# Optimization experiments

Hardware: AMD Instinct MI355X
Metric: run time of the kernel (lower is better)

The kernel has to match this reference:

```python
import jax, jax.numpy as jnp
import numpy as np

T, B, E, H = 2048, 4, 1024, 16
D = E // H  # head_dim = 64
SCALING = D ** -0.5


def setup_inputs() -> dict:
    key = jax.random.key(0)
    ks = jax.random.split(key, 5)
    w_scale = (2.0 / (E + E)) ** 0.5  # xavier_uniform-ish std
    return {
        "query": jax.random.normal(ks[0], (T, B, E), dtype=jnp.float32),
        "q_weight": jax.random.normal(ks[1], (E, E), dtype=jnp.float32) * w_scale,
        "k_weight": jax.random.normal(ks[2], (E, E), dtype=jnp.float32) * w_scale,
        "v_weight": jax.random.normal(ks[3], (E, E), dtype=jnp.float32) * w_scale,
        "out_proj_weight": jax.random.normal(ks[4], (E, E), dtype=jnp.float32) * w_scale,
        "q_bias": jnp.zeros((E,), dtype=jnp.float32),
        "k_bias": jnp.zeros((E,), dtype=jnp.float32),
        "v_bias": jnp.zeros((E,), dtype=jnp.float32),
        "out_proj_bias": jnp.zeros((E,), dtype=jnp.float32),
    }


def reference(query, q_weight, k_weight, v_weight, out_proj_weight,
              q_bias, k_bias, v_bias, out_proj_bias):
    # Linear projections: y = x @ W.T + b  (torch F.linear convention)
    q = jnp.einsum('tbe,fe->tbf', query, q_weight) + q_bias
    k = jnp.einsum('tbe,fe->tbf', query, k_weight) + k_bias
    v = jnp.einsum('tbe,fe->tbf', query, v_weight) + v_bias
    # split heads: [T, B, H, D]
    q = q.reshape(T, B, H, D) * SCALING
    k = k.reshape(T, B, H, D)
    v = v.reshape(T, B, H, D)
    # attention scores [B, H, T, T] over keys s
    scores = jnp.einsum('tbhd,sbhd->bhts', q, k)
    attn = jax.nn.softmax(scores, axis=-1)
    # context [T, B, H, D] -> [T, B, E]
    ctx = jnp.einsum('bhts,sbhd->tbhd', attn, v).reshape(T, B, E)
    # output projection
    out = jnp.einsum('tbe,fe->tbf', ctx, out_proj_weight) + out_proj_bias
    return out
```

## Files before the change

kernel.cpp:

```cpp
#include <hip/hip_runtime.h>
#include <hip/hip_bf16.h>
#include <stdint.h>

#define T_   2048
#define B_   4
#define E_   1024
#define H_   16
#define D_   64
#define M_   8192
#define KDIM 1024

using bf16 = __hip_bfloat16;
typedef __attribute__((ext_vector_type(8)))  short bf16x8;
typedef __attribute__((ext_vector_type(4)))  float f32x4;
typedef __attribute__((ext_vector_type(16))) float f32x16;

#define QK_SCALE 0.180336880f

#if __has_builtin(__builtin_amdgcn_exp2f)
#define EXP2F(x) __builtin_amdgcn_exp2f(x)
#else
#define EXP2F(x) exp2f(x)
#endif

__device__ __forceinline__ void gload_lds16(const void* g, void* l) {
  __builtin_amdgcn_global_load_lds(
      (const __attribute__((address_space(1))) void*)g,
      (__attribute__((address_space(3))) void*)l, 16, 0, 0);
}

__device__ __forceinline__ uint32_t pack_bf16(float lo, float hi) {
  union { __hip_bfloat162 h2; uint32_t u; } cv;
  cv.h2 = __float22bfloat162_rn(float2{lo, hi});
  return cv.u;
}

__device__ __forceinline__ void plswap(uint32_t& a, uint32_t& b) {
#if __has_builtin(__builtin_amdgcn_permlane32_swap)
  typedef __attribute__((ext_vector_type(2))) unsigned int u32x2_t;
  u32x2_t r = __builtin_amdgcn_permlane32_swap(a, b, false, false);
  a = r[0]; b = r[1];
#else
  asm volatile("v_permlane32_swap_b32 %0, %1" : "+v"(a), "+v"(b));
#endif
}
__device__ __forceinline__ float comb_add32(float x) {
  union { float f; uint32_t u; } a, b; a.f = x; b.f = x;
  plswap(a.u, b.u);
  return a.f + b.f;
}

__global__ void k_cvt_all(const float* __restrict__ X,
                          const float* __restrict__ Wq, const float* __restrict__ Wk,
                          const float* __restrict__ Wv, const float* __restrict__ Wo,
                          bf16* __restrict__ Xb,
                          bf16* __restrict__ Wqb, bf16* __restrict__ Wkb,
                          bf16* __restrict__ Wvb, bf16* __restrict__ Wob) {
  int id = blockIdx.x;
  const float* src; bf16* dst; int base;
  if (id < 8192) { src = X; dst = Xb; base = id; }
  else {
    int w = (id - 8192) >> 10;
    base = (id - 8192) & 1023;
    src = (w == 0) ? Wq : (w == 1) ? Wk : (w == 2) ? Wv : Wo;
    dst = (w == 0) ? Wqb : (w == 1) ? Wkb : (w == 2) ? Wvb : Wob;
  }
  int i = base * 256 + threadIdx.x;
  float4 v = reinterpret_cast<const float4*>(src)[i];
  bf16* d = dst + (size_t)i * 4;
  d[0] = __float2bfloat16(v.x);
  d[1] = __float2bfloat16(v.y);
  d[2] = __float2bfloat16(v.z);
  d[3] = __float2bfloat16(v.w);
}

__device__ __forceinline__ void gemm_tile_body(
    const bf16* __restrict__ A, const bf16* __restrict__ Bw,
    int bm, int bn, bf16* sA, bf16* sB, f32x4 (&acc)[4][4])
{
  const int t    = threadIdx.x;
  const int wave = t >> 6;
  const int lane = t & 63;
  const int l15  = lane & 15, l4 = lane >> 4;
  const int wr = wave >> 1, wc = wave & 1;
  const int srow = t >> 3;
  const int sg   = t & 7;

  for (int k0 = 0; k0 < KDIM; k0 += 64) {
#pragma unroll
    for (int rd = 0; rd < 4; ++rd) {
      int row = rd * 32 + srow;
      const bf16* src = A + (size_t)(bm * 128 + row) * KDIM + k0 + ((sg ^ (row & 7)) * 8);
      gload_lds16(src, sA + rd * 2048 + wave * 512);
    }
#pragma unroll
    for (int rd = 0; rd < 4; ++rd) {
      int row = rd * 32 + srow;
      const bf16* src = Bw + (size_t)(bn * 128 + row) * KDIM + k0 + ((sg ^ (row & 7)) * 8);
      gload_lds16(src, sB + rd * 2048 + wave * 512);
    }
    __syncthreads();

#pragma unroll
    for (int kk = 0; kk < 2; ++kk) {
      bf16x8 af[4], bfr[4];
#pragma unroll
      for (int m = 0; m < 4; ++m) {
        int row = wr * 64 + m * 16 + l15;
        int ch  = (l4 + kk * 4) ^ (row & 7);
        af[m] = *(const bf16x8*)(sA + row * 64 + ch * 8);
      }
#pragma unroll
      for (int n = 0; n < 4; ++n) {
        int row = wc * 64 + n * 16 + l15;
        int ch  = (l4 + kk * 4) ^ (row & 7);
        bfr[n] = *(const bf16x8*)(sB + row * 64 + ch * 8);
      }
#pragma unroll
      for (int m = 0; m < 4; ++m)
#pragma unroll
        for (int n = 0; n < 4; ++n)
          acc[m][n] = __builtin_amdgcn_mfma_f32_16x16x32_bf16(af[m], bfr[n], acc[m][n], 0, 0, 0);
    }
    __syncthreads();
  }
}

__global__ __launch_bounds__(256, 3) void k_gemm_qkv(
    const bf16* __restrict__ A,
    const bf16* __restrict__ Wq, const bf16* __restrict__ Wk, const bf16* __restrict__ Wv,
    const float* __restrict__ bq, const float* __restrict__ bk, const float* __restrict__ bv,
    bf16* __restrict__ outQ)
{
  __shared__ bf16 sA[128 * 64];
  __shared__ bf16 sB[128 * 64];
  const int bid = blockIdx.x;
  const int swz = (bid & 7) * 192 + (bid >> 3);
  const int bm = swz & 63;
  const int bn = swz >> 6;
  const int which = bn >> 3;
  const int bnn = bn & 7;
  const bf16* Bw = (which == 0) ? Wq : (which == 1) ? Wk : Wv;
  const float* bias = (which == 0) ? bq : (which == 1) ? bk : bv;
  const float scale = (which == 0) ? QK_SCALE : 1.0f;
  bf16* outb = outQ + (size_t)which * M_ * E_;

  f32x4 acc[4][4] = {};
  gemm_tile_body(A, Bw, bm, bnn, sA, sB, acc);

  const int lane = threadIdx.x & 63;
  const int l15 = lane & 15, l4 = lane >> 4;
  const int wave = threadIdx.x >> 6;
  const int wr = wave >> 1, wc = wave & 1;
#pragma unroll
  for (int m = 0; m < 4; ++m) {
#pragma unroll
    for (int n = 0; n < 4; ++n) {
      int gc = bnn * 128 + wc * 64 + n * 16 + l15;
      float bv_ = bias[gc];
#pragma unroll
      for (int r = 0; r < 4; ++r) {
        int gr = bm * 128 + wr * 64 + m * 16 + l4 * 4 + r;
        float v = (acc[m][n][r] + bv_) * scale;
        int tt = gr >> 2, bb = gr & 3;
        int hh = gc >> 6, dd = gc & 63;
        outb[(((size_t)(bb * H_ + hh)) * T_ + tt) * D_ + dd] = __float2bfloat16(v);
      }
    }
  }
}

__global__ __launch_bounds__(256, 3) void k_gemm_out(
    const bf16* __restrict__ A, const bf16* __restrict__ Bw,
    const float* __restrict__ bias, float* __restrict__ outf)
{
  __shared__ bf16 sA[128 * 64];
  __shared__ bf16 sB[128 * 64];
  const int bid = blockIdx.x;
  const int swz = (bid & 7) * 64 + (bid >> 3);
  const int bm = swz & 63;
  const int bn = swz >> 6;

  f32x4 acc[4][4] = {};
  gemm_tile_body(A, Bw, bm, bn, sA, sB, acc);

  const int lane = threadIdx.x & 63;
  const int l15 = lane & 15, l4 = lane >> 4;
  const int wave = threadIdx.x >> 6;
  const int wr = wave >> 1, wc = wave & 1;
#pragma unroll
  for (int m = 0; m < 4; ++m) {
#pragma unroll
    for (int n = 0; n < 4; ++n) {
      int gc = bn * 128 + wc * 64 + n * 16 + l15;
      float bv_ = bias[gc];
#pragma unroll
      for (int r = 0; r < 4; ++r) {
        int gr = bm * 128 + wr * 64 + m * 16 + l4 * 4 + r;
        outf[(size_t)gr * E_ + gc] = acc[m][n][r] + bv_;
      }
    }
  }
}

__global__ __launch_bounds__(256, 4) void k_attn5(
    const bf16* __restrict__ Qb, const bf16* __restrict__ Kb,
    const bf16* __restrict__ Vb, bf16* __restrict__ ctx)
{
  __shared__ bf16 sK [128 * 64];
  __shared__ bf16 sVT[2 * 64 * 64];

  const int t    = threadIdx.x;
  const int wave = t >> 6;
  const int lane = t & 63;
  const int l31  = lane & 31;
  const int h    = lane >> 5;

  const int bid = blockIdx.x;
  const int swz = (bid & 7) * 128 + (bid >> 3);
  const int bh  = swz >> 4;
  const int qt  = swz & 15;
  const int q0  = qt * 128;
  const size_t headoff = (size_t)bh * T_ * D_;

  const int qrow = q0 + wave * 32 + l31;
  bf16x8 qf[4];
#pragma unroll
  for (int kc = 0; kc < 4; ++kc)
    qf[kc] = *(const bf16x8*)(Qb + headoff + (size_t)qrow * 64 + kc * 16 + 8 * h);

  f32x16 acc0 = {}, acc1 = {};
  float lrun = 0.f;

  const int srow = t >> 3, sg = t & 7;
  const int vkey = (t >> 3) * 2, vd0 = (t & 7) * 8;

  for (int kt = 0; kt < T_ / 128; ++kt) {
    const bf16* ktile = Kb + headoff + (size_t)(kt * 128) * D_;
#pragma unroll
    for (int rd = 0; rd < 4; ++rd) {
      int row = rd * 32 + srow;
      gload_lds16(ktile + (size_t)row * 64 + ((sg ^ (row & 7)) * 8),
                  sK + rd * 2048 + wave * 512);
    }
#pragma unroll
    for (int s = 0; s < 2; ++s) {
      const bf16* vtile = Vb + headoff + (size_t)(kt * 128 + s * 64) * D_;
      bf16x8 va = *(const bf16x8*)(vtile + (size_t)vkey * 64 + vd0);
      bf16x8 vb = *(const bf16x8*)(vtile + (size_t)(vkey + 1) * 64 + vd0);
#pragma unroll
      for (int j = 0; j < 8; ++j) {
        int d = vd0 + j;
        int slot = (vkey >> 3) ^ (d & 7) ^ (d >> 3);
        uint32_t pk = (uint32_t)(uint16_t)va[j] | ((uint32_t)(uint16_t)vb[j] << 16);
        *reinterpret_cast<uint32_t*>(sVT + s * 4096 + d * 64 + slot * 8 + (vkey & 7)) = pk;
      }
    }
    __syncthreads();

#pragma unroll
    for (int s = 0; s < 2; ++s) {
      const bf16* sKs  = sK  + s * 64 * 64;
      const bf16* sVTs = sVT + s * 4096;

      f32x16 s0 = {}, s1 = {};
      __builtin_amdgcn_s_setprio(1);
#pragma unroll
      for (int kc = 0; kc < 4; ++kc) {
        int slot = ((2 * kc + h) ^ (l31 & 7)) * 8;
        bf16x8 a0 = *(const bf16x8*)(sKs + l31 * 64 + slot);
        bf16x8 a1 = *(const bf16x8*)(sKs + (32 + l31) * 64 + slot);
        s0 = __builtin_amdgcn_mfma_f32_32x32x16_bf16(a0, qf[kc], s0, 0, 0, 0);
        s1 = __builtin_amdgcn_mfma_f32_32x32x16_bf16(a1, qf[kc], s1, 0, 0, 0);
      }
      __builtin_amdgcn_s_setprio(0);

      float psum = 0.f;
#pragma unroll
      for (int r = 0; r < 16; ++r) { s0[r] = EXP2F(s0[r]); psum += s0[r]; }
#pragma unroll
      for (int r = 0; r < 16; ++r) { s1[r] = EXP2F(s1[r]); psum += s1[r]; }
      lrun += psum;

      uint32_t u[8][2];
#pragma unroll
      for (int g = 0; g < 4; ++g) {
        u[g][0]     = pack_bf16(s0[g * 4 + 0], s0[g * 4 + 1]);
        u[g][1]     = pack_bf16(s0[g * 4 + 2], s0[g * 4 + 3]);
        u[4 + g][0] = pack_bf16(s1[g * 4 + 0], s1[g * 4 + 1]);
        u[4 + g][1] = pack_bf16(s1[g * 4 + 2], s1[g * 4 + 3]);
      }

      bf16x8 pa[4];
#pragma unroll
      for (int ks = 0; ks < 4; ++ks) {
        uint32_t w0 = u[2 * ks][0], w2 = u[2 * ks + 1][0];
        uint32_t w1 = u[2 * ks][1], w3 = u[2 * ks + 1][1];
        plswap(w0, w2);
        plswap(w1, w3);
        union { uint32_t w[4]; bf16x8 v; } cv;
        cv.w[0] = w0; cv.w[1] = w1; cv.w[2] = w2; cv.w[3] = w3;
        pa[ks] = cv.v;
      }

      __builtin_amdgcn_s_setprio(1);
#pragma unroll
      for (int ks = 0; ks < 4; ++ks) {
        int d0 = l31, d1 = 32 + l31;
        bf16x8 v0 = *(const bf16x8*)(sVTs + d0 * 64 + (((2 * ks + h) ^ (d0 & 7) ^ (d0 >> 3)) * 8));
        bf16x8 v1 = *(const bf16x8*)(sVTs + d1 * 64 + (((2 * ks + h) ^ (d1 & 7) ^ (d1 >> 3)) * 8));
        acc0 = __builtin_amdgcn_mfma_f32_32x32x16_bf16(v0, pa[ks], acc0, 0, 0, 0);
        acc1 = __builtin_amdgcn_mfma_f32_32x32x16_bf16(v1, pa[ks], acc1, 0, 0, 0);
      }
      __builtin_amdgcn_s_setprio(0);
    }
    __syncthreads();
  }

  float lt = comb_add32(lrun);
  float rinv = 1.0f / lt;
  const int b = bh >> 4, hh = bh & 15;
#pragma unroll
  for (int dt = 0; dt < 2; ++dt) {
#pragma unroll
    for (int g = 0; g < 4; ++g) {
      float e0 = (dt ? acc1[g * 4 + 0] : acc0[g * 4 + 0]) * rinv;
      float e1 = (dt ? acc1[g * 4 + 1] : acc0[g * 4 + 1]) * rinv;
      float e2 = (dt ? acc1[g * 4 + 2] : acc0[g * 4 + 2]) * rinv;
      float e3 = (dt ? acc1[g * 4 + 3] : acc0[g * 4 + 3]) * rinv;
      int dbase = dt * 32 + g * 8 + 4 * h;
      uint2 wv = { pack_bf16(e0, e1), pack_bf16(e2, e3) };
      *reinterpret_cast<uint2*>(ctx + ((size_t)qrow * B_ + b) * E_ + hh * 64 + dbase) = wv;
    }
  }
}

extern "C" void kernel_launch(void* const* d_in, const int* in_sizes, int n_in,
                              void* d_out, int out_size, void* d_ws, size_t ws_size,
                              hipStream_t stream) {
  const float* X  = (const float*)d_in[0];
  const float* Wq = (const float*)d_in[1];
  const float* Wk = (const float*)d_in[2];
  const float* Wv = (const float*)d_in[3];
  const float* Wo = (const float*)d_in[4];
  const float* bq = (const float*)d_in[5];
  const float* bk = (const float*)d_in[6];
  const float* bv = (const float*)d_in[7];
  const float* bo = (const float*)d_in[8];
  float* out = (float*)d_out;

  char* ws = (char*)d_ws;
  const size_t XB   = (size_t)M_ * E_ * 2;
  const size_t WB   = (size_t)E_ * E_ * 2;
  bf16* Xb  = (bf16*)(ws);
  bf16* Wqb = (bf16*)(ws + XB);
  bf16* Wkb = (bf16*)(ws + XB + WB);
  bf16* Wvb = (bf16*)(ws + XB + 2 * WB);
  bf16* Wob = (bf16*)(ws + XB + 3 * WB);
  bf16* Qb  = (bf16*)(ws + XB + 4 * WB);
  bf16* Kb  = (bf16*)(ws + 2 * XB + 4 * WB);
  bf16* Vb  = (bf16*)(ws + 3 * XB + 4 * WB);
  bf16* Cx  = Xb;

  k_cvt_all<<<12288, 256, 0, stream>>>(X, Wq, Wk, Wv, Wo, Xb, Wqb, Wkb, Wvb, Wob);

  k_gemm_qkv<<<1536, 256, 0, stream>>>(Xb, Wqb, Wkb, Wvb, bq, bk, bv, Qb);

  k_attn5<<<1024, 256, 0, stream>>>(Qb, Kb, Vb, Cx);

  k_gemm_out<<<512, 256, 0, stream>>>(Cx, Wob, bo, out);
}
```

Measured before the change: 193.6 us.

## Fuse fp32-to-bf16 conversion of X into QKV GEMM A-tile loads

The separate conversion pass over the activation X is removed. The QKV GEMM now reads fp32 X directly, packs it to bf16 in registers and stores it to the swizzled shared-memory tile, while weights are still converted by a smaller kernel. This drops one write and one read of an 8192x1024 bf16 buffer. In exchange each X tile is re-read in fp32 by every column block (24 per row block), and the A loads become synchronous register loads instead of direct-to-LDS loads. The attention kernel also precomputes its swizzled LDS offsets outside the key loop to cut address arithmetic.

```diff
diff --git a/kernel.cpp b/kernel.cpp
--- a/kernel.cpp
+++ b/kernel.cpp
@@ -50,21 +50,14 @@
   return a.f + b.f;
 }
 
-__global__ void k_cvt_all(const float* __restrict__ X,
-                          const float* __restrict__ Wq, const float* __restrict__ Wk,
-                          const float* __restrict__ Wv, const float* __restrict__ Wo,
-                          bf16* __restrict__ Xb,
-                          bf16* __restrict__ Wqb, bf16* __restrict__ Wkb,
-                          bf16* __restrict__ Wvb, bf16* __restrict__ Wob) {
+__global__ void k_cvt_w(const float* __restrict__ Wq, const float* __restrict__ Wk,
+                        const float* __restrict__ Wv, const float* __restrict__ Wo,
+                        bf16* __restrict__ Wqb, bf16* __restrict__ Wkb,
+                        bf16* __restrict__ Wvb, bf16* __restrict__ Wob) {
   int id = blockIdx.x;
-  const float* src; bf16* dst; int base;
-  if (id < 8192) { src = X; dst = Xb; base = id; }
-  else {
-    int w = (id - 8192) >> 10;
-    base = (id - 8192) & 1023;
-    src = (w == 0) ? Wq : (w == 1) ? Wk : (w == 2) ? Wv : Wo;
-    dst = (w == 0) ? Wqb : (w == 1) ? Wkb : (w == 2) ? Wvb : Wob;
-  }
+  int w = id >> 10, base = id & 1023;
+  const float* src = (w == 0) ? Wq : (w == 1) ? Wk : (w == 2) ? Wv : Wo;
+  bf16* dst = (w == 0) ? Wqb : (w == 1) ? Wkb : (w == 2) ? Wvb : Wob;
   int i = base * 256 + threadIdx.x;
   float4 v = reinterpret_cast<const float4*>(src)[i];
   bf16* d = dst + (size_t)i * 4;
@@ -127,7 +120,7 @@
 }
 
 __global__ __launch_bounds__(256, 3) void k_gemm_qkv(
-    const bf16* __restrict__ A,
+    const float* __restrict__ Xf,
     const bf16* __restrict__ Wq, const bf16* __restrict__ Wk, const bf16* __restrict__ Wv,
     const float* __restrict__ bq, const float* __restrict__ bk, const float* __restrict__ bv,
     bf16* __restrict__ outQ)
@@ -145,13 +138,62 @@
   const float scale = (which == 0) ? QK_SCALE : 1.0f;
   bf16* outb = outQ + (size_t)which * M_ * E_;
 
+  const int t    = threadIdx.x;
+  const int wave = t >> 6;
+  const int lane = t & 63;
+  const int l15  = lane & 15, l4 = lane >> 4;
+  const int wr = wave >> 1, wc = wave & 1;
+  const int srow = t >> 3;
+  const int sg   = t & 7;
+
   f32x4 acc[4][4] = {};
-  gemm_tile_body(A, Bw, bm, bnn, sA, sB, acc);
-
-  const int lane = threadIdx.x & 63;
-  const int l15 = lane & 15, l4 = lane >> 4;
-  const int wave = threadIdx.x >> 6;
-  const int wr = wave >> 1, wc = wave & 1;
+
+  for (int k0 = 0; k0 < KDIM; k0 += 64) {
+#pragma unroll
+    for (int rd = 0; rd < 4; ++rd) {
+      int row = rd * 32 + srow;
+      const bf16* src = Bw + (size_t)(bnn * 128 + row) * KDIM + k0 + ((sg ^ (row & 7)) * 8);
+      gload_lds16(src, sB + rd * 2048 + wave * 512);
+    }
+#pragma unroll
+    for (int rd = 0; rd < 4; ++rd) {
+      int row = rd * 32 + srow;
+      const float4* xs = reinterpret_cast<const float4*>(
+          Xf + (size_t)(bm * 128 + row) * KDIM + k0 + ((sg ^ (row & 7)) * 8));
+      float4 f0 = xs[0], f1 = xs[1];
+      uint4 c;
+      c.x = pack_bf16(f0.x, f0.y);
+      c.y = pack_bf16(f0.z, f0.w);
+      c.z = pack_bf16(f1.x, f1.y);
+      c.w = pack_bf16(f1.z, f1.w);
+      *reinterpret_cast<uint4*>(sA + rd * 2048 + wave * 512 + lane * 8) = c;
+    }
+    __syncthreads();
+
+#pragma unroll
+    for (int kk = 0; kk < 2; ++kk) {
+      bf16x8 af[4], bfr[4];
+#pragma unroll
+      for (int m = 0; m < 4; ++m) {
+        int row = wr * 64 + m * 16 + l15;
+        int ch  = (l4 + kk * 4) ^ (row & 7);
+        af[m] = *(const bf16x8*)(sA + row * 64 + ch * 8);
+      }
+#pragma unroll
+      for (int n = 0; n < 4; ++n) {
+        int row = wc * 64 + n * 16 + l15;
+        int ch  = (l4 + kk * 4) ^ (row & 7);
+        bfr[n] = *(const bf16x8*)(sB + row * 64 + ch * 8);
+      }
+#pragma unroll
+      for (int m = 0; m < 4; ++m)
+#pragma unroll
+        for (int n = 0; n < 4; ++n)
+          acc[m][n] = __builtin_amdgcn_mfma_f32_16x16x32_bf16(af[m], bfr[n], acc[m][n], 0, 0, 0);
+    }
+    __syncthreads();
+  }
+
 #pragma unroll
   for (int m = 0; m < 4; ++m) {
 #pragma unroll
@@ -235,13 +277,33 @@
   const int srow = t >> 3, sg = t & 7;
   const int vkey = (t >> 3) * 2, vd0 = (t & 7) * 8;
 
+  int off_qk[4][2];
+#pragma unroll
+  for (int kc = 0; kc < 4; ++kc) {
+    int slot = ((2 * kc + h) ^ (l31 & 7)) * 8;
+    off_qk[kc][0] = l31 * 64 + slot;
+    off_qk[kc][1] = (32 + l31) * 64 + slot;
+  }
+  int off_pv[4][2];
+#pragma unroll
+  for (int ks = 0; ks < 4; ++ks) {
+    int d0 = l31, d1 = 32 + l31;
+    off_pv[ks][0] = d0 * 64 + (((2 * ks + h) ^ (d0 & 7) ^ (d0 >> 3)) * 8);
+    off_pv[ks][1] = d1 * 64 + (((2 * ks + h) ^ (d1 & 7) ^ (d1 >> 3)) * 8);
+  }
+  int off_vw[8];
+#pragma unroll
+  for (int j = 0; j < 8; ++j) {
+    int d = vd0 + j;
+    off_vw[j] = d * 64 + (((vkey >> 3) ^ (d & 7) ^ (d >> 3)) * 8) + (vkey & 7);
+  }
+  const int koff = srow * 64 + ((sg ^ (srow & 7)) * 8);
+
   for (int kt = 0; kt < T_ / 128; ++kt) {
     const bf16* ktile = Kb + headoff + (size_t)(kt * 128) * D_;
 #pragma unroll
     for (int rd = 0; rd < 4; ++rd) {
-      int row = rd * 32 + srow;
-      gload_lds16(ktile + (size_t)row * 64 + ((sg ^ (row & 7)) * 8),
-                  sK + rd * 2048 + wave * 512);
+      gload_lds16(ktile + (size_t)rd * 2048 + koff, sK + rd * 2048 + wave * 512);
     }
 #pragma unroll
     for (int s = 0; s < 2; ++s) {
@@ -250,26 +312,20 @@
       bf16x8 vb = *(const bf16x8*)(vtile + (size_t)(vkey + 1) * 64 + vd0);
 #pragma unroll
       for (int j = 0; j < 8; ++j) {
-        int d = vd0 + j;
-        int slot = (vkey >> 3) ^ (d & 7) ^ (d >> 3);
         uint32_t pk = (uint32_t)(uint16_t)va[j] | ((uint32_t)(uint16_t)vb[j] << 16);
-        *reinterpret_cast<uint32_t*>(sVT + s * 4096 + d * 64 + slot * 8 + (vkey & 7)) = pk;
+        *reinterpret_cast<uint32_t*>(sVT + s * 4096 + off_vw[j]) = pk;
       }
     }
     __syncthreads();
 
 #pragma unroll
     for (int s = 0; s < 2; ++s) {
-      const bf16* sKs  = sK  + s * 64 * 64;
-      const bf16* sVTs = sVT + s * 4096;
-
       f32x16 s0 = {}, s1 = {};
       __builtin_amdgcn_s_setprio(1);
 #pragma unroll
       for (int kc = 0; kc < 4; ++kc) {
-        int slot = ((2 * kc + h) ^ (l31 & 7)) * 8;
-        bf16x8 a0 = *(const bf16x8*)(sKs + l31 * 64 + slot);
-        bf16x8 a1 = *(const bf16x8*)(sKs + (32 + l31) * 64 + slot);
+        bf16x8 a0 = *(const bf16x8*)(sK + s * 4096 + off_qk[kc][0]);
+        bf16x8 a1 = *(const bf16x8*)(sK + s * 4096 + off_qk[kc][1]);
         s0 = __builtin_amdgcn_mfma_f32_32x32x16_bf16(a0, qf[kc], s0, 0, 0, 0);
         s1 = __builtin_amdgcn_mfma_f32_32x32x16_bf16(a1, qf[kc], s1, 0, 0, 0);
       }
@@ -306,9 +362,8 @@
       __builtin_amdgcn_s_setprio(1);
 #pragma unroll
       for (int ks = 0; ks < 4; ++ks) {
-        int d0 = l31, d1 = 32 + l31;
-        bf16x8 v0 = *(const bf16x8*)(sVTs + d0 * 64 + (((2 * ks + h) ^ (d0 & 7) ^ (d0 >> 3)) * 8));
-        bf16x8 v1 = *(const bf16x8*)(sVTs + d1 * 64 + (((2 * ks + h) ^ (d1 & 7) ^ (d1 >> 3)) * 8));
+        bf16x8 v0 = *(const bf16x8*)(sVT + s * 4096 + off_pv[ks][0]);
+        bf16x8 v1 = *(const bf16x8*)(sVT + s * 4096 + off_pv[ks][1]);
         acc0 = __builtin_amdgcn_mfma_f32_32x32x16_bf16(v0, pa[ks], acc0, 0, 0, 0);
         acc1 = __builtin_amdgcn_mfma_f32_32x32x16_bf16(v1, pa[ks], acc1, 0, 0, 0);
       }
@@ -352,7 +407,6 @@
   char* ws = (char*)d_ws;
   const size_t XB   = (size_t)M_ * E_ * 2;
   const size_t WB   = (size_t)E_ * E_ * 2;
-  bf16* Xb  = (bf16*)(ws);
   bf16* Wqb = (bf16*)(ws + XB);
   bf16* Wkb = (bf16*)(ws + XB + WB);
   bf16* Wvb = (bf16*)(ws + XB + 2 * WB);
@@ -360,11 +414,11 @@
   bf16* Qb  = (bf16*)(ws + XB + 4 * WB);
   bf16* Kb  = (bf16*)(ws + 2 * XB + 4 * WB);
   bf16* Vb  = (bf16*)(ws + 3 * XB + 4 * WB);
-  bf16* Cx  = Xb;
-
-  k_cvt_all<<<12288, 256, 0, stream>>>(X, Wq, Wk, Wv, Wo, Xb, Wqb, Wkb, Wvb, Wob);
-
-  k_gemm_qkv<<<1536, 256, 0, stream>>>(Xb, Wqb, Wkb, Wvb, bq, bk, bv, Qb);
+  bf16* Cx  = (bf16*)(ws);
+
+  k_cvt_w<<<4096, 256, 0, stream>>>(Wq, Wk, Wv, Wo, Wqb, Wkb, Wvb, Wob);
+
+  k_gemm_qkv<<<1536, 256, 0, stream>>>(X, Wqb, Wkb, Wvb, bq, bk, bv, Qb);
 
   k_attn5<<<1024, 256, 0, stream>>>(Qb, Kb, Vb, Cx);
 
```

After: 236.7 us. 22.2% more time.
